# Kernel tuning notes

Hardware: AMD Instinct MI355X
Metric: run time of the kernel (lower is better)

## Reference

```python
import jax, jax.numpy as jnp
import numpy as np

B, T, D, H = 64, 512, 300, 256
K1, K2 = 10, 12


def lstm(x, mask, W, b):
    # x: [B,T,Din], mask: [B,T] bool. TF LSTMCell gate order i,j,f,o; forget_bias=1.0.
    xT = jnp.swapaxes(x, 0, 1)  # [T,B,Din]
    mT = jnp.swapaxes(mask, 0, 1)  # [T,B]
    Hd = b.shape[0] // 4
    Bn = x.shape[0]

    def step(carry, inp):
        h, c = carry
        xt, mt = inp
        z = jnp.concatenate([xt, h], axis=-1) @ W + b
        i, j, f, o = jnp.split(z, 4, axis=-1)
        c_new = jax.nn.sigmoid(f + 1.0) * c + jax.nn.sigmoid(i) * jnp.tanh(j)
        h_new = jax.nn.sigmoid(o) * jnp.tanh(c_new)
        m = mt[:, None]
        c2 = jnp.where(m, c_new, c)
        h2 = jnp.where(m, h_new, h)
        out = jnp.where(m, h_new, jnp.zeros_like(h_new))  # dynamic_rnn zeros past length
        return (h2, c2), out

    init = (jnp.zeros((Bn, Hd), x.dtype), jnp.zeros((Bn, Hd), x.dtype))
    _, outs = jax.lax.scan(step, init, (xT, mT))
    return jnp.swapaxes(outs, 0, 1)  # [B,T,H]


def reverse_seq(x, lengths):
    # reverse each sequence along time up to its length (padding stays in place)
    t = jnp.arange(x.shape[1])
    idx = lengths[:, None] - 1 - t[None, :]
    idx = jnp.where(idx >= 0, idx, t[None, :])
    return jnp.take_along_axis(x, idx[:, :, None], axis=1)


def bilstm(x, lengths, mask, Wf, bf, Wb, bb):
    fw = lstm(x, mask, Wf, bf)
    xr = reverse_seq(x, lengths)
    bw = reverse_seq(lstm(xr, mask, Wb, bb), lengths)
    return jnp.concatenate([fw, bw], axis=-1)  # [B,T,2H]


def crf_nll(logits, labels, lengths, trans):
    # negative crf_log_likelihood per example
    Tn = logits.shape[1]
    t = jnp.arange(Tn)
    mask = t[None, :] < lengths[:, None]  # [B,T]
    unary = jnp.take_along_axis(logits, labels[:, :, None], 2)[:, :, 0]
    unary_score = jnp.sum(jnp.where(mask, unary, 0.0), axis=1)
    tr = trans[labels[:, :-1], labels[:, 1:]]
    trans_score = jnp.sum(jnp.where(mask[:, 1:], tr, 0.0), axis=1)

    def step(alpha, inp):
        lt, mt = inp  # [B,K], [B]
        new = jax.nn.logsumexp(alpha[:, :, None] + trans[None, :, :], axis=1) + lt
        return jnp.where(mt[:, None], new, alpha), None

    alpha, _ = jax.lax.scan(
        step, logits[:, 0],
        (jnp.swapaxes(logits[:, 1:], 0, 1), jnp.swapaxes(mask[:, 1:], 0, 1)))
    logZ = jax.nn.logsumexp(alpha, axis=-1)
    return logZ - (unary_score + trans_score)


def setup_inputs() -> dict:
    key = jax.random.key(0)
    ks = jax.random.split(key, 24)
    s = 0.05
    inp = {
        'embedded_words': jax.random.normal(ks[0], (B, T, D), jnp.float32),
        'sentence_lenghts': jax.random.randint(ks[1], (B,), 1, T + 1, jnp.int32),
        'labels': jax.random.randint(ks[2], (B, T), 0, K1, jnp.int32),
    }
    i = 3
    for scope in ('t1', 't2', 'sh'):
        for d in ('fw', 'bw'):
            inp[f'{scope}_{d}_W'] = jax.random.normal(ks[i], (D + H, 4 * H), jnp.float32) * s
            inp[f'{scope}_{d}_b'] = jnp.zeros((4 * H,), jnp.float32)
            i += 1
    inp['W1'] = jax.random.normal(ks[i], (4 * H, K1), jnp.float32) * s; i += 1
    inp['b1'] = jnp.zeros((K1,), jnp.float32)
    inp['W2'] = jax.random.normal(ks[i], (4 * H, K2), jnp.float32) * s; i += 1
    inp['b2'] = jnp.zeros((K2,), jnp.float32)
    inp['trans1'] = jax.random.normal(ks[i], (K1, K1), jnp.float32) * s; i += 1
    inp['trans2'] = jax.random.normal(ks[i], (K2, K2), jnp.float32) * s
    return inp


def reference(embedded_words, sentence_lenghts, labels,
              t1_fw_W, t1_fw_b, t1_bw_W, t1_bw_b,
              t2_fw_W, t2_fw_b, t2_bw_W, t2_bw_b,
              sh_fw_W, sh_fw_b, sh_bw_W, sh_bw_b,
              W1, b1, W2, b2, trans1, trans2):
    mask = jnp.arange(embedded_words.shape[1])[None, :] < sentence_lenghts[:, None]
    t1 = bilstm(embedded_words, sentence_lenghts, mask, t1_fw_W, t1_fw_b, t1_bw_W, t1_bw_b)
    t2 = bilstm(embedded_words, sentence_lenghts, mask, t2_fw_W, t2_fw_b, t2_bw_W, t2_bw_b)
    sh = bilstm(embedded_words, sentence_lenghts, mask, sh_fw_W, sh_fw_b, sh_bw_W, sh_bw_b)
    logits1 = jnp.concatenate([t1, sh], axis=-1) @ W1 + b1  # [B,T,K1]
    logits2 = jnp.concatenate([t2, sh], axis=-1) @ W2 + b2  # [B,T,K2]
    nll1 = crf_nll(logits1, labels, sentence_lenghts, trans1)
    nll2 = crf_nll(logits2, labels, sentence_lenghts, trans2)
    return jnp.stack([nll1, nll2])  # [2,B]
```

## Files before the change

kernel.cpp:

```cpp
#include <hip/hip_runtime.h>
#include <cstdint>
#include <cstddef>

#define B_ 64
#define T_ 512
#define D_ 300
#define DP_ 320
#define H_ 256
#define G4_ 1024
#define NL_ 6

typedef float f32x4 __attribute__((ext_vector_type(4)));
typedef __bf16 bf16x8 __attribute__((ext_vector_type(8)));

struct WPtrs { const float* W[NL_]; const float* Bv[NL_]; };

__device__ __forceinline__ unsigned short f2bf(float f){
  unsigned int u = __float_as_uint(f);
  unsigned int r = u + 0x7FFFu + ((u >> 16) & 1u);
  return (unsigned short)(r >> 16);
}
__device__ __forceinline__ float bf2f(unsigned int s){
  return __uint_as_float((s & 0xFFFFu) << 16);
}
__device__ __forceinline__ float fast_sig(float x){
  return __builtin_amdgcn_rcpf(1.f + __builtin_amdgcn_exp2f(-1.4426950408889634f * x));
}
__device__ __forceinline__ float fast_tanh(float x){
  return 1.f - 2.f * __builtin_amdgcn_rcpf(1.f + __builtin_amdgcn_exp2f(2.8853900817779268f * x));
}
__device__ __forceinline__ void store8bf(unsigned short* p, const unsigned short v[8]){
  uint4 u;
  u.x = (unsigned)v[0] | ((unsigned)v[1] << 16);
  u.y = (unsigned)v[2] | ((unsigned)v[3] << 16);
  u.z = (unsigned)v[4] | ((unsigned)v[5] << 16);
  u.w = (unsigned)v[6] | ((unsigned)v[7] << 16);
  *(uint4*)p = u;
}

__global__ void k_prep_x(const float* __restrict__ x, const int* __restrict__ len,
                         unsigned short* __restrict__ xb, unsigned short* __restrict__ xrb){
  int idx = blockIdx.x * 256 + threadIdx.x;
  int d8 = idx % 40;
  int bt = idx / 40;
  if (bt >= B_ * T_) return;
  int t = bt & (T_ - 1);
  int b = bt >> 9;
  int L = len[b];
  int tdst = (t < L) ? (L - 1 - t) : t;
  const float* xs = x + (size_t)bt * D_;
  unsigned short v[8];
  #pragma unroll
  for (int e = 0; e < 8; e++){
    int d = d8 * 8 + e;
    v[e] = f2bf(d < D_ ? xs[d] : 0.f);
  }
  store8bf(xb + (size_t)bt * DP_ + d8 * 8, v);
  store8bf(xrb + ((size_t)b * T_ + tdst) * DP_ + d8 * 8, v);
}

__global__ void k_prep_w(WPtrs wp, unsigned short* __restrict__ whp,
                         unsigned short* __restrict__ wxp,
                         const float* __restrict__ W1, const float* __restrict__ W2,
                         float* __restrict__ w1t, float* __restrict__ w2t){
  int idx = blockIdx.x * 256 + threadIdx.x;
  const int nWh = NL_ * 16 * 4 * 8 * 64;
  const int nWx = NL_ * 16 * 10 * 4 * 64;
  if (idx < nWh){
    int lane = idx & 63, kt = (idx >> 6) & 7, g = (idx >> 9) & 3, s = (idx >> 11) & 15, l = idx >> 15;
    int col = g * 256 + s * 16 + (lane & 15);
    int k0 = kt * 32 + (lane >> 4) * 8;
    const float* W = wp.W[l];
    unsigned short v[8];
    #pragma unroll
    for (int e = 0; e < 8; e++) v[e] = f2bf(W[(size_t)(D_ + k0 + e) * G4_ + col]);
    store8bf(whp + ((((size_t)(l * 16 + s) * 4 + g) * 8 + kt) * 64 + lane) * 8, v);
  } else if (idx < nWh + nWx){
    int i2 = idx - nWh;
    int lane = i2 & 63;
    int g = (i2 >> 6) & 3;
    int r = i2 >> 8;
    int kt = r % 10;
    int r2 = r / 10;
    int s = r2 & 15, l = r2 >> 4;
    int col = g * 256 + s * 16 + (lane & 15);
    int k0 = kt * 32 + (lane >> 4) * 8;
    const float* W = wp.W[l];
    unsigned short v[8];
    #pragma unroll
    for (int e = 0; e < 8; e++){
      int k = k0 + e;
      v[e] = f2bf(k < D_ ? W[(size_t)k * G4_ + col] : 0.f);
    }
    store8bf(wxp + ((((size_t)(l * 16 + s) * 10 + kt) * 4 + g) * 64 + lane) * 8, v);
  } else if (idx < nWh + nWx + 16384){
    int i2 = idx - nWh - nWx;
    int h = i2 & 1023, k = i2 >> 10;
    w1t[k * G4_ + h] = (k < 10) ? W1[h * 10 + k] : 0.f;
  } else if (idx < nWh + nWx + 32768){
    int i2 = idx - nWh - nWx - 16384;
    int h = i2 & 1023, k = i2 >> 10;
    w2t[k * G4_ + h] = (k < 12) ? W2[h * 12 + k] : 0.f;
  }
}

__global__ __launch_bounds__(256, 1) void k_rec(
    const unsigned short* __restrict__ whp, const unsigned short* __restrict__ wxp,
    const unsigned short* __restrict__ xb, const unsigned short* __restrict__ xrb,
    WPtrs wp, const int* __restrict__ len,
    unsigned short* __restrict__ hbuf, int* __restrict__ cnt,
    unsigned short* __restrict__ ho){
  int l = blockIdx.x & 7;
  if (l >= NL_) return;
  int s = blockIdx.x >> 3;
  int tid = threadIdx.x, lane = tid & 63, w = tid >> 6;
  const int isbw = l & 1;
  const unsigned short* xsrc = isbw ? xrb : xb;

  bf16x8 Bh[4][8];
  #pragma unroll
  for (int g = 0; g < 4; g++)
    #pragma unroll
    for (int kt = 0; kt < 8; kt++)
      Bh[g][kt] = *(const bf16x8*)(whp + ((((size_t)(l * 16 + s) * 4 + g) * 8 + kt) * 64 + lane) * 8);

  float bias[4];
  #pragma unroll
  for (int g = 0; g < 4; g++) bias[g] = wp.Bv[l][g * 256 + s * 16 + (lane & 15)];

  float c4[4] = {0.f, 0.f, 0.f, 0.f};
  float h4[4] = {0.f, 0.f, 0.f, 0.f};
  int Lr[4];
  #pragma unroll
  for (int r = 0; r < 4; r++) Lr[r] = len[w * 16 + (lane >> 4) * 4 + r];

  int hcol = s * 16 + (lane & 15);
  int arow = w * 16 + (lane & 15);
  int* flag = cnt + l * T_;
  const unsigned short* xrow = xsrc + (size_t)arow * T_ * DP_ + (lane >> 4) * 8;
  const unsigned short* wxs = wxp + (size_t)(l * 16 + s) * 10 * 4 * 64 * 8 + (size_t)lane * 8;
  unsigned short* hb[2];
  hb[0] = hbuf + ((size_t)(0 * NL_ + l) * B_) * H_;
  hb[1] = hbuf + ((size_t)(1 * NL_ + l) * B_) * H_;

  union U16x8 { unsigned long long q[2]; bf16x8 v; };

  for (int t = 0; t < T_; t++){
    f32x4 acc[4];
    #pragma unroll
    for (int g = 0; g < 4; g++){ acc[g].x = 0.f; acc[g].y = 0.f; acc[g].z = 0.f; acc[g].w = 0.f; }
    const unsigned short* xt = xrow + (size_t)t * DP_;
    #pragma unroll
    for (int kt = 0; kt < 10; kt++){
      bf16x8 Ax = *(const bf16x8*)(xt + kt * 32);
      #pragma unroll
      for (int g = 0; g < 4; g++){
        bf16x8 Bx = *(const bf16x8*)(wxs + ((size_t)(kt * 4 + g) * 64) * 8);
        acc[g] = __builtin_amdgcn_mfma_f32_16x16x32_bf16(Ax, Bx, acc[g], 0, 0, 0);
      }
    }
    const unsigned short* hrow = hb[(t + 1) & 1] + (size_t)arow * H_ + (lane >> 4) * 8;
    bf16x8 Ah[8];
    #pragma unroll
    for (int kt = 0; kt < 8; kt++){
      U16x8 u;
      u.q[0] = __hip_atomic_load((const unsigned long long*)(hrow + kt * 32), __ATOMIC_RELAXED, __HIP_MEMORY_SCOPE_AGENT);
      u.q[1] = __hip_atomic_load((const unsigned long long*)(hrow + kt * 32) + 1, __ATOMIC_RELAXED, __HIP_MEMORY_SCOPE_AGENT);
      Ah[kt] = u.v;
    }
    if (t > 0){
      int f = __hip_atomic_load(&flag[t - 1], __ATOMIC_RELAXED, __HIP_MEMORY_SCOPE_AGENT);
      if (f < 16){
        if (lane == 0){
          int gd = 0;
          while (__hip_atomic_load(&flag[t - 1], __ATOMIC_RELAXED, __HIP_MEMORY_SCOPE_AGENT) < 16){
            __builtin_amdgcn_s_sleep(1);
            if (++gd > (1 << 15)) break;
          }
        }
        #pragma unroll
        for (int kt = 0; kt < 8; kt++){
          U16x8 u;
          u.q[0] = __hip_atomic_load((const unsigned long long*)(hrow + kt * 32), __ATOMIC_RELAXED, __HIP_MEMORY_SCOPE_AGENT);
          u.q[1] = __hip_atomic_load((const unsigned long long*)(hrow + kt * 32) + 1, __ATOMIC_RELAXED, __HIP_MEMORY_SCOPE_AGENT);
          Ah[kt] = u.v;
        }
      }
    }
    #pragma unroll
    for (int kt = 0; kt < 8; kt++)
      #pragma unroll
      for (int g = 0; g < 4; g++)
        acc[g] = __builtin_amdgcn_mfma_f32_16x16x32_bf16(Ah[kt], Bh[g][kt], acc[g], 0, 0, 0);

    unsigned short hpub[4], hov[4];
    #pragma unroll
    for (int r = 0; r < 4; r++){
      float gi = acc[0][r] + bias[0], gj = acc[1][r] + bias[1];
      float gf = acc[2][r] + bias[2], go = acc[3][r] + bias[3];
      float cn = fast_sig(gf + 1.f) * c4[r] + fast_sig(gi) * fast_tanh(gj);
      float hn = fast_sig(go) * fast_tanh(cn);
      bool m = (t < Lr[r]);
      c4[r] = m ? cn : c4[r];
      h4[r] = m ? hn : h4[r];
      hpub[r] = f2bf(h4[r]);
      hov[r] = f2bf(m ? hn : 0.f);
    }
    unsigned short* hdst = hb[t & 1] + hcol;
    #pragma unroll
    for (int r = 0; r < 4; r++){
      int b = w * 16 + (lane >> 4) * 4 + r;
      __hip_atomic_store(hdst + (size_t)b * H_, hpub[r], __ATOMIC_RELAXED, __HIP_MEMORY_SCOPE_AGENT);
    }
    asm volatile("s_waitcnt vmcnt(0)" ::: "memory");
    __syncthreads();
    if (tid == 0)
      __hip_atomic_fetch_add(&flag[t], 1, __ATOMIC_RELAXED, __HIP_MEMORY_SCOPE_AGENT);
    #pragma unroll
    for (int r = 0; r < 4; r++){
      int b = w * 16 + (lane >> 4) * 4 + r;
      int tdst = isbw ? ((t < Lr[r]) ? (Lr[r] - 1 - t) : t) : t;
      ho[(((size_t)b * T_ + tdst) * NL_ + l) * H_ + hcol] = hov[r];
    }
  }
}

__global__ void k_logits(const unsigned short* __restrict__ ho,
                         const float* __restrict__ w1t, const float* __restrict__ w2t,
                         const float* __restrict__ b1, const float* __restrict__ b2,
                         float* __restrict__ lgt){
  int gid = blockIdx.x * 4 + (threadIdx.x >> 6);
  int lane = threadIdx.x & 63;
  const unsigned short* hrow = ho + (size_t)gid * (NL_ * H_);
  float hv[6][4];
  #pragma unroll
  for (int lgi = 0; lgi < 6; lgi++){
    uint2 u = *(const uint2*)(hrow + lgi * H_ + lane * 4);
    hv[lgi][0] = bf2f(u.x); hv[lgi][1] = bf2f(u.x >> 16);
    hv[lgi][2] = bf2f(u.y); hv[lgi][3] = bf2f(u.y >> 16);
  }
  float s1[10], s2[12];
  #pragma unroll
  for (int k = 0; k < 10; k++) s1[k] = 0.f;
  #pragma unroll
  for (int k = 0; k < 12; k++) s2[k] = 0.f;
  const int seg1[4] = {0, 1, 4, 5};
  const int seg2[4] = {2, 3, 4, 5};
  #pragma unroll
  for (int k = 0; k < 10; k++){
    #pragma unroll
    for (int ii = 0; ii < 4; ii++){
      float4 wv = *(const float4*)(w1t + k * G4_ + ii * 256 + lane * 4);
      int lgi = seg1[ii];
      s1[k] += hv[lgi][0] * wv.x + hv[lgi][1] * wv.y + hv[lgi][2] * wv.z + hv[lgi][3] * wv.w;
    }
  }
  #pragma unroll
  for (int k = 0; k < 12; k++){
    #pragma unroll
    for (int ii = 0; ii < 4; ii++){
      float4 wv = *(const float4*)(w2t + k * G4_ + ii * 256 + lane * 4);
      int lgi = seg2[ii];
      s2[k] += hv[lgi][0] * wv.x + hv[lgi][1] * wv.y + hv[lgi][2] * wv.z + hv[lgi][3] * wv.w;
    }
  }
  #pragma unroll
  for (int k = 0; k < 10; k++)
    #pragma unroll
    for (int d = 1; d < 64; d <<= 1) s1[k] += __shfl_xor(s1[k], d, 64);
  #pragma unroll
  for (int k = 0; k < 12; k++)
    #pragma unroll
    for (int d = 1; d < 64; d <<= 1) s2[k] += __shfl_xor(s2[k], d, 64);
  if (lane == 0){
    int b = gid >> 9, t = gid & 511;
    float* o1 = lgt + ((size_t)(0 * B_ + b) * T_ + t) * 16;
    float* o2 = lgt + ((size_t)(1 * B_ + b) * T_ + t) * 16;
    #pragma unroll
    for (int k = 0; k < 10; k++) o1[k] = s1[k] + b1[k];
    #pragma unroll
    for (int k = 0; k < 12; k++) o2[k] = s2[k] + b2[k];
  }
}

__global__ void k_crf(const float* __restrict__ lgt, const int* __restrict__ labels,
                      const int* __restrict__ len, const float* __restrict__ trans1,
                      const float* __restrict__ trans2, float* __restrict__ out){
  int gid = blockIdx.x * 4 + (threadIdx.x >> 6);
  int lane = threadIdx.x & 63;
  int tau = gid >> 6;
  int b = gid & 63;
  int K = tau ? 12 : 10;
  const float* tr = tau ? trans2 : trans1;
  const float* lgp = lgt + (size_t)(tau * B_ + b) * T_ * 16;
  int L = len[b];
  int k2 = lane & 15;
  const float LOG2E = 1.4426950408889634f;
  const float LN2 = 0.6931471805599453f;
  float Et[12];
  #pragma unroll
  for (int k1 = 0; k1 < 12; k1++)
    Et[k1] = (k1 < K && k2 < K) ? __builtin_amdgcn_exp2f(LOG2E * tr[k1 * K + k2]) : 0.f;
  float alpha = (k2 < K) ? lgp[k2] : -1e30f;
  for (int t = 1; t < L; t++){
    float m = alpha;
    #pragma unroll
    for (int d = 1; d < 16; d <<= 1) m = fmaxf(m, __shfl_xor(m, d, 16));
    float e = __builtin_amdgcn_exp2f(LOG2E * (alpha - m));
    float ss = 0.f;
    #pragma unroll
    for (int k1 = 0; k1 < 12; k1++)
      ss += __shfl(e, k1, 16) * Et[k1];
    float na = m + LN2 * __builtin_amdgcn_logf(ss) + lgp[t * 16 + k2];
    alpha = (k2 < K) ? na : -1e30f;
  }
  float m2 = alpha;
  #pragma unroll
  for (int d = 1; d < 16; d <<= 1) m2 = fmaxf(m2, __shfl_xor(m2, d, 16));
  float e2 = __builtin_amdgcn_exp2f(LOG2E * (alpha - m2));
  #pragma unroll
  for (int d = 1; d < 16; d <<= 1) e2 += __shfl_xor(e2, d, 16);
  float logZ = m2 + LN2 * __builtin_amdgcn_logf(e2);
  float us = 0.f;
  const int* lab = labels + b * T_;
  for (int t0 = lane; t0 < L; t0 += 64){
    int la = lab[t0];
    us += lgp[t0 * 16 + la];
    if (t0 >= 1) us += tr[lab[t0 - 1] * K + la];
  }
  #pragma unroll
  for (int d = 1; d < 64; d <<= 1) us += __shfl_xor(us, d, 64);
  if (lane == 0) out[tau * B_ + b] = logZ - us;
}

extern "C" void kernel_launch(void* const* d_in, const int* in_sizes, int n_in,
                              void* d_out, int out_size, void* d_ws, size_t ws_size,
                              hipStream_t stream){
  const float* x = (const float*)d_in[0];
  const int* len = (const int*)d_in[1];
  const int* labels = (const int*)d_in[2];
  WPtrs wp;
  for (int l = 0; l < NL_; l++){
    wp.W[l] = (const float*)d_in[3 + 2 * l];
    wp.Bv[l] = (const float*)d_in[4 + 2 * l];
  }
  const float* W1 = (const float*)d_in[15];
  const float* b1 = (const float*)d_in[16];
  const float* W2 = (const float*)d_in[17];
  const float* b2 = (const float*)d_in[18];
  const float* trans1 = (const float*)d_in[19];
  const float* trans2 = (const float*)d_in[20];

  char* ws = (char*)d_ws;
  const size_t SZ_HB  = 2ull * NL_ * B_ * H_ * 2;
  const size_t SZ_CNT = (size_t)NL_ * T_ * 4;
  const size_t O_XB  = SZ_HB + SZ_CNT;
  const size_t SZ_X  = (size_t)B_ * T_ * DP_ * 2;
  const size_t O_XRB = O_XB + SZ_X;
  const size_t O_WHP = O_XRB + SZ_X;
  const size_t SZ_WHP = (size_t)NL_ * H_ * G4_ * 2;
  const size_t O_WXP = O_WHP + SZ_WHP;
  const size_t SZ_WXP = (size_t)NL_ * DP_ * G4_ * 2;
  const size_t O_W1T = O_WXP + SZ_WXP;
  const size_t O_W2T = O_W1T + 65536;
  const size_t O_HO  = O_W2T + 65536;
  const size_t SZ_HO = (size_t)B_ * T_ * NL_ * H_ * 2;
  const size_t O_LGT = O_HO + SZ_HO;

  unsigned short* hbuf = (unsigned short*)(ws + 0);
  int* cnt = (int*)(ws + SZ_HB);
  unsigned short* xb  = (unsigned short*)(ws + O_XB);
  unsigned short* xrb = (unsigned short*)(ws + O_XRB);
  unsigned short* whp = (unsigned short*)(ws + O_WHP);
  unsigned short* wxp = (unsigned short*)(ws + O_WXP);
  float* w1t = (float*)(ws + O_W1T);
  float* w2t = (float*)(ws + O_W2T);
  unsigned short* ho = (unsigned short*)(ws + O_HO);
  float* lgt = (float*)(ws + O_LGT);

  hipMemsetAsync(ws, 0, SZ_HB + SZ_CNT, stream);
  k_prep_x<<<5120, 256, 0, stream>>>(x, len, xb, xrb);
  k_prep_w<<<1856, 256, 0, stream>>>(wp, whp, wxp, W1, W2, w1t, w2t);
  k_rec<<<128, 256, 0, stream>>>(whp, wxp, xb, xrb, wp, len, hbuf, cnt, ho);
  k_logits<<<8192, 256, 0, stream>>>(ho, w1t, w2t, b1, b2, lgt);
  k_crf<<<32, 256, 0, stream>>>(lgt, labels, len, trans1, trans2, (float*)d_out);
}
```

Measured before the change: 3.128 ms.

## Replace per-step counter barrier with timestep-tagged hidden state and register-resident input weights

The recurrent kernel drops the per-step __syncthreads and flag counter. Each published hidden value is now a 32-bit word whose high half carries the timestep tag, and consumers spin until every tag they read matches, which removes the block barrier and the extra flag round trip. Input-projection weights are now held in registers, the input sequence is pre-laid out in MFMA fragment order for both directions, and the grid drops from 128 to 96 blocks. The cost is twice the hidden-state traffic plus heavy register pressure from keeping Bx[10][4] alongside Bh. Spinning on tags also relies on relaxed atomic ordering being enough for correctness.

```diff
diff --git a/kernel.cpp b/kernel.cpp
--- a/kernel.cpp
+++ b/kernel.cpp
@@ -39,24 +39,28 @@
 }
 
 __global__ void k_prep_x(const float* __restrict__ x, const int* __restrict__ len,
-                         unsigned short* __restrict__ xb, unsigned short* __restrict__ xrb){
+                         unsigned short* __restrict__ xf){
   int idx = blockIdx.x * 256 + threadIdx.x;
-  int d8 = idx % 40;
-  int bt = idx / 40;
-  if (bt >= B_ * T_) return;
-  int t = bt & (T_ - 1);
-  int b = bt >> 9;
-  int L = len[b];
-  int tdst = (t < L) ? (L - 1 - t) : t;
-  const float* xs = x + (size_t)bt * D_;
+  int lane = idx & 63;
+  int kt = (idx >> 6) % 10;
+  int r1 = idx / 640;
+  int bt = r1 & 3;
+  int r2 = r1 >> 2;
+  int t = r2 & 511;
+  int dir = r2 >> 9;
+  if (dir >= 2) return;
+  int bb = bt * 16 + (lane & 15);
+  int k0 = kt * 32 + (lane >> 4) * 8;
+  int L = len[bb];
+  int tsrc = dir ? ((t < L) ? (L - 1 - t) : t) : t;
+  const float* xs = x + ((size_t)bb * T_ + tsrc) * D_;
   unsigned short v[8];
   #pragma unroll
   for (int e = 0; e < 8; e++){
-    int d = d8 * 8 + e;
-    v[e] = f2bf(d < D_ ? xs[d] : 0.f);
-  }
-  store8bf(xb + (size_t)bt * DP_ + d8 * 8, v);
-  store8bf(xrb + ((size_t)b * T_ + tdst) * DP_ + d8 * 8, v);
+    int k = k0 + e;
+    v[e] = f2bf(k < D_ ? xs[k] : 0.f);
+  }
+  store8bf(xf + ((size_t)idx) * 8, v);
 }
 
 __global__ void k_prep_w(WPtrs wp, unsigned short* __restrict__ whp,
@@ -104,18 +108,35 @@
   }
 }
 
+#define LOADH_BLOCK() \
+  { _Pragma("unroll") \
+    for (int kt = 0; kt < 8; kt++){ \
+      const unsigned long long* hq64 = (const unsigned long long*)(hsrc + kt * 32 + (lane >> 4) * 8); \
+      _Pragma("unroll") \
+      for (int j = 0; j < 4; j++) \
+        hq[kt][j] = __hip_atomic_load(hq64 + j, __ATOMIC_RELAXED, __HIP_MEMORY_SCOPE_AGENT); \
+    } }
+
+#define CHECKH_BLOCK(okv, tg) \
+  { okv = true; \
+    _Pragma("unroll") \
+    for (int kt = 0; kt < 8; kt++){ \
+      _Pragma("unroll") \
+      for (int j = 0; j < 4; j++){ \
+        unsigned lo = (unsigned)hq[kt][j]; \
+        unsigned hi = (unsigned)(hq[kt][j] >> 32); \
+        okv = okv && ((lo >> 16) == tg) && ((hi >> 16) == tg); \
+      } \
+    } }
+
 __global__ __launch_bounds__(256, 1) void k_rec(
     const unsigned short* __restrict__ whp, const unsigned short* __restrict__ wxp,
-    const unsigned short* __restrict__ xb, const unsigned short* __restrict__ xrb,
-    WPtrs wp, const int* __restrict__ len,
-    unsigned short* __restrict__ hbuf, int* __restrict__ cnt,
-    unsigned short* __restrict__ ho){
-  int l = blockIdx.x & 7;
-  if (l >= NL_) return;
-  int s = blockIdx.x >> 3;
+    const unsigned short* __restrict__ xf, WPtrs wp, const int* __restrict__ len,
+    unsigned int* __restrict__ hpub, unsigned short* __restrict__ ho){
+  int l = blockIdx.x >> 4;
+  int s = blockIdx.x & 15;
   int tid = threadIdx.x, lane = tid & 63, w = tid >> 6;
-  const int isbw = l & 1;
-  const unsigned short* xsrc = isbw ? xrb : xb;
+  const int dir = l & 1;
 
   bf16x8 Bh[4][8];
   #pragma unroll
@@ -123,6 +144,12 @@
     #pragma unroll
     for (int kt = 0; kt < 8; kt++)
       Bh[g][kt] = *(const bf16x8*)(whp + ((((size_t)(l * 16 + s) * 4 + g) * 8 + kt) * 64 + lane) * 8);
+  bf16x8 Bx[10][4];
+  #pragma unroll
+  for (int kt = 0; kt < 10; kt++)
+    #pragma unroll
+    for (int g = 0; g < 4; g++)
+      Bx[kt][g] = *(const bf16x8*)(wxp + ((((size_t)(l * 16 + s) * 10 + kt) * 4 + g) * 64 + lane) * 8);
 
   float bias[4];
   #pragma unroll
@@ -134,66 +161,54 @@
   #pragma unroll
   for (int r = 0; r < 4; r++) Lr[r] = len[w * 16 + (lane >> 4) * 4 + r];
 
-  int hcol = s * 16 + (lane & 15);
+  int unit = s * 16 + (lane & 15);
   int arow = w * 16 + (lane & 15);
-  int* flag = cnt + l * T_;
-  const unsigned short* xrow = xsrc + (size_t)arow * T_ * DP_ + (lane >> 4) * 8;
-  const unsigned short* wxs = wxp + (size_t)(l * 16 + s) * 10 * 4 * 64 * 8 + (size_t)lane * 8;
-  unsigned short* hb[2];
-  hb[0] = hbuf + ((size_t)(0 * NL_ + l) * B_) * H_;
-  hb[1] = hbuf + ((size_t)(1 * NL_ + l) * B_) * H_;
-
-  union U16x8 { unsigned long long q[2]; bf16x8 v; };
+  unsigned int* hp0 = hpub + ((size_t)(l * 2 + 0) * B_) * H_;
+  unsigned int* hp1 = hpub + ((size_t)(l * 2 + 1) * B_) * H_;
 
   for (int t = 0; t < T_; t++){
+    unsigned long long hq[8][4];
+    const unsigned int* hsrc = ((t & 1) ? hp0 : hp1) + (size_t)arow * H_;
+    if (t > 0){
+      LOADH_BLOCK();
+    }
     f32x4 acc[4];
     #pragma unroll
     for (int g = 0; g < 4; g++){ acc[g].x = 0.f; acc[g].y = 0.f; acc[g].z = 0.f; acc[g].w = 0.f; }
-    const unsigned short* xt = xrow + (size_t)t * DP_;
+    const unsigned short* xt = xf + (((size_t)(dir * T_ + t) * 4 + w) * 10) * 512;
     #pragma unroll
     for (int kt = 0; kt < 10; kt++){
-      bf16x8 Ax = *(const bf16x8*)(xt + kt * 32);
+      bf16x8 Ax = *(const bf16x8*)(xt + (size_t)kt * 512 + lane * 8);
       #pragma unroll
-      for (int g = 0; g < 4; g++){
-        bf16x8 Bx = *(const bf16x8*)(wxs + ((size_t)(kt * 4 + g) * 64) * 8);
-        acc[g] = __builtin_amdgcn_mfma_f32_16x16x32_bf16(Ax, Bx, acc[g], 0, 0, 0);
+      for (int g = 0; g < 4; g++)
+        acc[g] = __builtin_amdgcn_mfma_f32_16x16x32_bf16(Ax, Bx[kt][g], acc[g], 0, 0, 0);
+    }
+    if (t > 0){
+      unsigned tg = (unsigned)(t - 1);
+      bool ok;
+      CHECKH_BLOCK(ok, tg);
+      int tries = 0;
+      while (!__all(ok) && ++tries < 8192){
+        LOADH_BLOCK();
+        CHECKH_BLOCK(ok, tg);
       }
-    }
-    const unsigned short* hrow = hb[(t + 1) & 1] + (size_t)arow * H_ + (lane >> 4) * 8;
-    bf16x8 Ah[8];
-    #pragma unroll
-    for (int kt = 0; kt < 8; kt++){
-      U16x8 u;
-      u.q[0] = __hip_atomic_load((const unsigned long long*)(hrow + kt * 32), __ATOMIC_RELAXED, __HIP_MEMORY_SCOPE_AGENT);
-      u.q[1] = __hip_atomic_load((const unsigned long long*)(hrow + kt * 32) + 1, __ATOMIC_RELAXED, __HIP_MEMORY_SCOPE_AGENT);
-      Ah[kt] = u.v;
-    }
-    if (t > 0){
-      int f = __hip_atomic_load(&flag[t - 1], __ATOMIC_RELAXED, __HIP_MEMORY_SCOPE_AGENT);
-      if (f < 16){
-        if (lane == 0){
-          int gd = 0;
-          while (__hip_atomic_load(&flag[t - 1], __ATOMIC_RELAXED, __HIP_MEMORY_SCOPE_AGENT) < 16){
-            __builtin_amdgcn_s_sleep(1);
-            if (++gd > (1 << 15)) break;
-          }
+      #pragma unroll
+      for (int kt = 0; kt < 8; kt++){
+        union { unsigned u[4]; bf16x8 v; } uu;
+        #pragma unroll
+        for (int j = 0; j < 4; j++){
+          unsigned lo = (unsigned)hq[kt][j];
+          unsigned hi = (unsigned)(hq[kt][j] >> 32);
+          uu.u[j] = (lo & 0xFFFFu) | (hi << 16);
         }
         #pragma unroll
-        for (int kt = 0; kt < 8; kt++){
-          U16x8 u;
-          u.q[0] = __hip_atomic_load((const unsigned long long*)(hrow + kt * 32), __ATOMIC_RELAXED, __HIP_MEMORY_SCOPE_AGENT);
-          u.q[1] = __hip_atomic_load((const unsigned long long*)(hrow + kt * 32) + 1, __ATOMIC_RELAXED, __HIP_MEMORY_SCOPE_AGENT);
-          Ah[kt] = u.v;
-        }
+        for (int g = 0; g < 4; g++)
+          acc[g] = __builtin_amdgcn_mfma_f32_16x16x32_bf16(uu.v, Bh[g][kt], acc[g], 0, 0, 0);
       }
     }
-    #pragma unroll
-    for (int kt = 0; kt < 8; kt++)
-      #pragma unroll
-      for (int g = 0; g < 4; g++)
-        acc[g] = __builtin_amdgcn_mfma_f32_16x16x32_bf16(Ah[kt], Bh[g][kt], acc[g], 0, 0, 0);
-
-    unsigned short hpub[4], hov[4];
+    unsigned int* hdst = ((t & 1) ? hp1 : hp0) + unit;
+    unsigned short hov[4];
+    unsigned tagt = ((unsigned)t) << 16;
     #pragma unroll
     for (int r = 0; r < 4; r++){
       float gi = acc[0][r] + bias[0], gj = acc[1][r] + bias[1];
@@ -203,24 +218,16 @@
       bool m = (t < Lr[r]);
       c4[r] = m ? cn : c4[r];
       h4[r] = m ? hn : h4[r];
-      hpub[r] = f2bf(h4[r]);
       hov[r] = f2bf(m ? hn : 0.f);
-    }
-    unsigned short* hdst = hb[t & 1] + hcol;
+      int b = w * 16 + (lane >> 4) * 4 + r;
+      __hip_atomic_store(hdst + (size_t)b * H_, tagt | (unsigned)f2bf(h4[r]),
+                         __ATOMIC_RELAXED, __HIP_MEMORY_SCOPE_AGENT);
+    }
     #pragma unroll
     for (int r = 0; r < 4; r++){
       int b = w * 16 + (lane >> 4) * 4 + r;
-      __hip_atomic_store(hdst + (size_t)b * H_, hpub[r], __ATOMIC_RELAXED, __HIP_MEMORY_SCOPE_AGENT);
-    }
-    asm volatile("s_waitcnt vmcnt(0)" ::: "memory");
-    __syncthreads();
-    if (tid == 0)
-      __hip_atomic_fetch_add(&flag[t], 1, __ATOMIC_RELAXED, __HIP_MEMORY_SCOPE_AGENT);
-    #pragma unroll
-    for (int r = 0; r < 4; r++){
-      int b = w * 16 + (lane >> 4) * 4 + r;
-      int tdst = isbw ? ((t < Lr[r]) ? (Lr[r] - 1 - t) : t) : t;
-      ho[(((size_t)b * T_ + tdst) * NL_ + l) * H_ + hcol] = hov[r];
+      int tdst = dir ? ((t < Lr[r]) ? (Lr[r] - 1 - t) : t) : t;
+      ho[(((size_t)b * T_ + tdst) * NL_ + l) * H_ + unit] = hov[r];
     }
   }
 }
@@ -352,36 +359,33 @@
   const float* trans2 = (const float*)d_in[20];
 
   char* ws = (char*)d_ws;
-  const size_t SZ_HB  = 2ull * NL_ * B_ * H_ * 2;
-  const size_t SZ_CNT = (size_t)NL_ * T_ * 4;
-  const size_t O_XB  = SZ_HB + SZ_CNT;
-  const size_t SZ_X  = (size_t)B_ * T_ * DP_ * 2;
-  const size_t O_XRB = O_XB + SZ_X;
-  const size_t O_WHP = O_XRB + SZ_X;
+  const size_t SZ_HPUB = 2ull * NL_ * B_ * H_ * 4;
+  const size_t O_WHP = SZ_HPUB;
   const size_t SZ_WHP = (size_t)NL_ * H_ * G4_ * 2;
   const size_t O_WXP = O_WHP + SZ_WHP;
   const size_t SZ_WXP = (size_t)NL_ * DP_ * G4_ * 2;
-  const size_t O_W1T = O_WXP + SZ_WXP;
-  const size_t O_W2T = O_W1T + 65536;
-  const size_t O_HO  = O_W2T + 65536;
+  const size_t O_XF  = O_WXP + SZ_WXP;
+  const size_t SZ_XF = 2ull * T_ * 4 * 10 * 64 * 8 * 2;
+  const size_t O_HO  = O_XF + SZ_XF;
   const size_t SZ_HO = (size_t)B_ * T_ * NL_ * H_ * 2;
   const size_t O_LGT = O_HO + SZ_HO;
-
-  unsigned short* hbuf = (unsigned short*)(ws + 0);
-  int* cnt = (int*)(ws + SZ_HB);
-  unsigned short* xb  = (unsigned short*)(ws + O_XB);
-  unsigned short* xrb = (unsigned short*)(ws + O_XRB);
+  const size_t SZ_LGT = 2ull * B_ * T_ * 16 * 4;
+  const size_t O_W1T = O_LGT + SZ_LGT;
+  const size_t O_W2T = O_W1T + 65536;
+
+  unsigned int* hpub = (unsigned int*)(ws + 0);
   unsigned short* whp = (unsigned short*)(ws + O_WHP);
   unsigned short* wxp = (unsigned short*)(ws + O_WXP);
+  unsigned short* xf  = (unsigned short*)(ws + O_XF);
+  unsigned short* ho  = (unsigned short*)(ws + O_HO);
+  float* lgt = (float*)(ws + O_LGT);
   float* w1t = (float*)(ws + O_W1T);
   float* w2t = (float*)(ws + O_W2T);
-  unsigned short* ho = (unsigned short*)(ws + O_HO);
-  float* lgt = (float*)(ws + O_LGT);
-
-  hipMemsetAsync(ws, 0, SZ_HB + SZ_CNT, stream);
-  k_prep_x<<<5120, 256, 0, stream>>>(x, len, xb, xrb);
+
+  hipMemsetAsync(hpub, 0xFF, SZ_HPUB, stream);
+  k_prep_x<<<10240, 256, 0, stream>>>(x, len, xf);
   k_prep_w<<<1856, 256, 0, stream>>>(wp, whp, wxp, W1, W2, w1t, w2t);
-  k_rec<<<128, 256, 0, stream>>>(whp, wxp, xb, xrb, wp, len, hbuf, cnt, ho);
+  k_rec<<<96, 256, 0, stream>>>(whp, wxp, xf, wp, len, hpub, ho);
   k_logits<<<8192, 256, 0, stream>>>(ho, w1t, w2t, b1, b2, lgt);
   k_crf<<<32, 256, 0, stream>>>(lgt, labels, len, trans1, trans2, (float*)d_out);
 }
```

Measured after the change: 5.089 ms. 62.7% more time.
